# Performance work log

Hardware: AMD Instinct MI355X
Metric: run time of the kernel (lower is better)

The kernel has to match this reference:

```python
import jax, jax.numpy as jnp
import numpy as np

LN_EPS = 1e-5  # torch.nn.LayerNorm default

def g(x):
    # minGRU activation: x + 0.5 for x >= 0, sigmoid(x) otherwise (always positive)
    return jnp.where(x >= 0, x + 0.5, jax.nn.sigmoid(x))

def log_g(x):
    return jnp.where(x >= 0, jnp.log(jax.nn.relu(x) + 0.5), -jax.nn.softplus(-x))

def layernorm(x, gamma, beta):
    mu = jnp.mean(x, axis=-1, keepdims=True)
    var = jnp.var(x, axis=-1, keepdims=True)
    return (x - mu) * jax.lax.rsqrt(var + LN_EPS) * gamma + beta

def mingru_scan(gate, hidden, h0):
    # gate, hidden: (B,S,D); h0: (B,1,D) positive
    # z = sigmoid(gate); h_t = (1-z_t)*h_{t-1} + z_t * g(hidden_t)
    # evaluated via Heinsen parallel scan in log space
    log_z = -jax.nn.softplus(-gate)          # log sigmoid(gate)
    log_coeffs = -jax.nn.softplus(gate)      # log(1 - sigmoid(gate))
    log_h0 = jnp.log(h0)                     # (B,1,D)
    log_tilde_h = log_g(hidden)
    a_star = jnp.cumsum(
        jnp.concatenate([jnp.zeros_like(log_h0), log_coeffs], axis=1), axis=1
    )                                        # (B,S+1,D)
    log_vals = jnp.concatenate([log_h0, log_z + log_tilde_h], axis=1) - a_star
    log_h = a_star + jax.lax.cumlogsumexp(log_vals, axis=1)
    return jnp.exp(log_h)[:, 1:]             # (B,S,D)

def setup_inputs() -> dict:
    key = jax.random.key(0)
    k1, k2 = jax.random.split(key)
    B, S, D, L = 8, 4096, 1024, 3
    x = jax.random.normal(k1, (B, S, D), dtype=jnp.float32)
    W = jax.random.normal(k2, (L, D, 2 * D), dtype=jnp.float32) * 0.02
    b = jnp.zeros((L, 2 * D), dtype=jnp.float32)
    ln_gamma = jnp.ones((L, D), dtype=jnp.float32)
    ln_beta = jnp.zeros((L, D), dtype=jnp.float32)
    return {"x": x, "ln_gamma": ln_gamma, "ln_beta": ln_beta, "W": W, "b": b}

def reference(x, ln_gamma, ln_beta, W, b):
    B, S, D = x.shape
    L = W.shape[0]
    inp = x
    next_hidden = []
    for l in range(L):
        h_prev = jnp.full((B, 1, D), 0.5, dtype=x.dtype)  # g(zeros) = 0.5
        xn = layernorm(inp, ln_gamma[l], ln_beta[l])
        gh = jnp.einsum('bsd,de->bse', xn, W[l]) + b[l]   # (B,S,2D)
        gate, hidden = jnp.split(gh, 2, axis=2)
        out = mingru_scan(gate, hidden, h_prev)
        next_hidden.append(out[:, -1:])
        out = out + inp  # residual (sizes equal -> identity res_align)
        inp = out
    return (out, *next_hidden)
```

## Files before the change

kernel.cpp:

```cpp
#include <hip/hip_runtime.h>

typedef unsigned short u16;
typedef unsigned int   u32;
typedef float  f32x2  __attribute__((ext_vector_type(2)));
typedef float  f32x4  __attribute__((ext_vector_type(4)));
typedef short  bf16x8 __attribute__((ext_vector_type(8)));
typedef u16    u16x4  __attribute__((ext_vector_type(4)));
typedef u32    u32x4  __attribute__((ext_vector_type(4)));

#define BQ 8
#define SQ 4096
#define DQ 1024
#define NQ 2048
#define MQ 32768
#define KQ 1024
#define CCH 128
#define TCH 32
#define NT 16

__device__ __forceinline__ float bf2f(u16 u){
  union { u32 i; float f; } v; v.i = ((u32)u) << 16; return v.f;
}
__device__ __forceinline__ u16 f2bf(float f){
  union { float f; u32 i; } v; v.f = f;
  u32 r = v.i + 0x7fffu + ((v.i >> 16) & 1u);
  return (u16)(r >> 16);
}

__device__ __forceinline__ void sig_ab(float gate, float hid, float& a, float& bv){
  float eg = __expf(gate);
  float a_ = __builtin_amdgcn_rcpf(1.f + eg);
  float z  = 1.f - a_;
  float eh = __expf(hid);
  float sg = eh * __builtin_amdgcn_rcpf(1.f + eh);
  float gval = (hid >= 0.f) ? (hid + 0.5f) : sg;
  a = a_; bv = z * gval;
}

__device__ __forceinline__ void gload_lds16(const u16* g, u16* l){
  __builtin_amdgcn_global_load_lds(
      (const __attribute__((address_space(1))) u32*)g,
      (__attribute__((address_space(3)))       u32*)l,
      16, 0, 0);
}

__global__ __launch_bounds__(256) void wt_cast(const float* __restrict__ W,
                                               u16* __restrict__ WT){
  __shared__ float t[64][65];
  const int l  = blockIdx.z;
  const int k0 = blockIdx.x << 6, n0 = blockIdx.y << 6;
  const float* Wl = W  + (size_t)l * KQ * NQ;
  u16*         Tl = WT + (size_t)l * NQ * KQ;
  const int c = threadIdx.x & 63, r4 = threadIdx.x >> 6;
  #pragma unroll
  for (int i = 0; i < 16; ++i){
    int r = i * 4 + r4;
    t[r][c] = Wl[(size_t)(k0 + r) * NQ + n0 + c];
  }
  __syncthreads();
  #pragma unroll
  for (int i = 0; i < 16; ++i){
    int r = i * 4 + r4;
    Tl[(size_t)(n0 + r) * KQ + k0 + c] = f2bf(t[c][r]);
  }
}

__global__ __launch_bounds__(256) void ln_cast(const float* __restrict__ x,
                                               const float* __restrict__ gamma,
                                               const float* __restrict__ beta,
                                               u16* __restrict__ xn){
  const size_t row = blockIdx.x;
  const int tid = threadIdx.x;
  f32x4 xv = *(const f32x4*)(x + row * DQ + tid * 4);
  float s  = xv[0] + xv[1] + xv[2] + xv[3];
  float s2 = xv[0]*xv[0] + xv[1]*xv[1] + xv[2]*xv[2] + xv[3]*xv[3];
  #pragma unroll
  for (int off = 32; off > 0; off >>= 1){
    s  += __shfl_down(s,  off);
    s2 += __shfl_down(s2, off);
  }
  __shared__ float red[8];
  const int wave = tid >> 6, lane = tid & 63;
  if (lane == 0){ red[wave] = s; red[4 + wave] = s2; }
  __syncthreads();
  s  = red[0] + red[1] + red[2] + red[3];
  s2 = red[4] + red[5] + red[6] + red[7];
  const float mean = s * (1.f / DQ);
  float var = fmaxf(s2 * (1.f / DQ) - mean * mean, 0.f);
  const float rstd = rsqrtf(var + 1e-5f);
  f32x4 gv = *(const f32x4*)(gamma + tid * 4);
  f32x4 bv = *(const f32x4*)(beta  + tid * 4);
  u16x4 o;
  #pragma unroll
  for (int e = 0; e < 4; ++e) o[e] = f2bf((xv[e] - mean) * rstd * gv[e] + bv[e]);
  *(u16x4*)(xn + row * DQ + tid * 4) = o;
}

__global__ __launch_bounds__(512, 2) void gemm_k8(const u16* __restrict__ A,
                                                  const u16* __restrict__ Bt,
                                                  const float* __restrict__ bias,
                                                  u32* __restrict__ abv,
                                                  float* __restrict__ pq){
  __shared__ u16 lds[2][2][2][8192];
  const int bid = blockIdx.x;
  const int swz = ((bid & 7) << 7) | (bid >> 3);
  const int bn = swz & 7, bm = swz >> 3;
  const int m0 = bm << 8;
  const int tid = threadIdx.x;
  const int w = tid >> 6, lane = tid & 63;
  const int wr = w >> 2, wc = w & 3;
  const int lr = lane & 15, hi = lane >> 4;
  const int sl8 = lane >> 3;
  const int sslot = (lane & 7) ^ sl8;

  f32x4 acc[2][2][4][2] = {};
  bf16x8 afrA[4][2], afrB[4][2];
  bf16x8 bf0[2][2], bf1[2][2];

#define FENCE asm volatile("" ::: "memory")
#define BAR do { FENCE; __builtin_amdgcn_s_barrier(); FENCE; } while(0)
#define SB  __builtin_amdgcn_sched_barrier(0)

#define STAGE(op, hf, kt, pb_) do {                                            \
    const u16* gsrc_ = (op) ? Bt : A;                                          \
    const int rb_ = (op) ? ((bn << 7) + (hf) * 1024) : (m0 + ((hf) << 7));     \
    _Pragma("unroll")                                                          \
    for (int g_ = 0; g_ < 2; ++g_){                                            \
      const int row_ = (w << 4) + (g_ << 3) + sl8;                             \
      gload_lds16(gsrc_ + (size_t)(rb_ + row_) * KQ + ((kt) << 6) + (sslot << 3),\
                  &lds[pb_][op][hf][((w << 4) + (g_ << 3)) << 6]);             \
    }                                                                          \
  } while(0)

#define LDSRD(dst, base_, row_, slot_) do {                                    \
    const int r_ = (row_);                                                     \
    dst = *(const bf16x8*)((const char*)(base_) +                              \
          ((r_ << 7) + ((((slot_)) ^ (r_ & 7)) << 4)));                        \
  } while(0)

#define RD_A(dst, hf, buf_) do {                                               \
    const u16* Ah_ = &lds[buf_][0][hf][0];                                     \
    _Pragma("unroll")                                                          \
    for (int i_ = 0; i_ < 4; ++i_)                                             \
      _Pragma("unroll")                                                        \
      for (int kk_ = 0; kk_ < 2; ++kk_)                                        \
        LDSRD(dst[i_][kk_], Ah_, (wr << 6) + (i_ << 4) + lr, (kk_ << 2) + hi); \
  } while(0)

#define RD_B(dst, hf, buf_) do {                                               \
    const u16* Bh_ = &lds[buf_][1][hf][0];                                     \
    _Pragma("unroll")                                                          \
    for (int j_ = 0; j_ < 2; ++j_)                                             \
      _Pragma("unroll")                                                        \
      for (int kk_ = 0; kk_ < 2; ++kk_)                                        \
        LDSRD(dst[j_][kk_], Bh_, (wc << 5) + (j_ << 4) + lr, (kk_ << 2) + hi); \
  } while(0)

#define MM(qm, qn, AR, B) do {                                                 \
    SB;                                                                        \
    __builtin_amdgcn_s_setprio(1);                                             \
    _Pragma("unroll")                                                          \
    for (int kk_ = 0; kk_ < 2; ++kk_)                                          \
      _Pragma("unroll")                                                        \
      for (int i_ = 0; i_ < 4; ++i_)                                           \
        _Pragma("unroll")                                                      \
        for (int j_ = 0; j_ < 2; ++j_)                                         \
          acc[qm][qn][i_][j_] = __builtin_amdgcn_mfma_f32_16x16x32_bf16(       \
              AR[i_][kk_], B[j_][kk_], acc[qm][qn][i_][j_], 0, 0, 0);          \
    __builtin_amdgcn_s_setprio(0);                                             \
  } while(0)

  STAGE(1, 0, 0, 0); STAGE(0, 0, 0, 0); STAGE(1, 1, 0, 0); STAGE(0, 1, 0, 0);
  asm volatile("s_waitcnt vmcnt(4)" ::: "memory");
  BAR;
  RD_A(afrA, 0, 0); RD_B(bf0, 0, 0);

  for (int t = 0; t < NT; ++t){
    const int pb = t & 1, qb = pb ^ 1;
    const bool s = (t + 1 < NT);
    asm volatile("s_waitcnt vmcnt(2)" ::: "memory");
    BAR;
    if (s) STAGE(1, 0, t + 1, qb);
    RD_B(bf1, 1, pb);
    MM(0, 0, afrA, bf0);
    if (s) { asm volatile("s_waitcnt vmcnt(2)" ::: "memory"); }
    else   { asm volatile("s_waitcnt vmcnt(0)" ::: "memory"); }
    BAR;
    if (s) STAGE(0, 0, t + 1, qb);
    RD_A(afrB, 1, pb);
    MM(0, 1, afrA, bf1);
    if (s) STAGE(1, 1, t + 1, qb);
    MM(1, 0, afrB, bf0);
    if (s){
      asm volatile("s_waitcnt vmcnt(2)" ::: "memory");
      BAR;
      STAGE(0, 1, t + 1, qb);
      RD_A(afrA, 0, qb); RD_B(bf0, 0, qb);
    }
    MM(1, 1, afrB, bf1);
  }
#undef MM
#undef RD_B
#undef RD_A
#undef LDSRD
#undef STAGE
#undef SB

  const int dbase = (bn << 7) + (wc << 5) + lr;
  #pragma unroll
  for (int qm = 0; qm < 2; ++qm){
    const int row00 = m0 + (qm << 7) + (wr << 6);
    #pragma unroll
    for (int half = 0; half < 2; ++half){
      float chP[2] = {1.f, 1.f}, chQ[2] = {0.f, 0.f};
      #pragma unroll
      for (int ii = 0; ii < 2; ++ii){
        const int i = (half << 1) + ii;
        float sgP[2] = {1.f, 1.f}, sgQ[2] = {0.f, 0.f};
        #pragma unroll
        for (int r = 0; r < 4; ++r){
          const int row = row00 + (i << 4) + (hi << 2) + r;
          #pragma unroll
          for (int j = 0; j < 2; ++j){
            const int d = dbase + (j << 4);
            float gate = acc[qm][0][i][j][r] + bias[d];
            float hid  = acc[qm][1][i][j][r] + bias[1024 + d];
            float a, bv; sig_ab(gate, hid, a, bv);
            u32 pk;
            asm volatile("v_cvt_pk_bf16_f32 %0, %1, %2"
                         : "=v"(pk) : "v"(a), "v"(bv));
            abv[(size_t)row * 1024 + d] = pk;
            union { u32 u; float f; } ua, ub;
            ua.u = pk << 16; ub.u = pk & 0xffff0000u;
            sgQ[j] = ua.f * sgQ[j] + ub.f;
            sgP[j] *= ua.f;
          }
        }
        #pragma unroll
        for (int j = 0; j < 2; ++j){
          float p = sgP[j], q = sgQ[j];
          float p1 = __shfl_up(p, 16), q1 = __shfl_up(q, 16);
          if (hi >= 1){ q = p * q1 + q; p = p * p1; }
          float p2 = __shfl_up(p, 32), q2 = __shfl_up(q, 32);
          if (hi >= 2){ q = p * q2 + q; p = p * p2; }
          chQ[j] = p * chQ[j] + q;
          chP[j] = p * chP[j];
        }
      }
      if (hi == 3){
        const int rowb = row00 + (half << 5);
        const int bq = rowb >> 12, cq = (rowb >> 5) & (CCH - 1);
        #pragma unroll
        for (int j = 0; j < 2; ++j){
          const int d = dbase + (j << 4);
          f32x2 v; v[0] = chP[j]; v[1] = chQ[j];
          *(f32x2*)(pq + ((((size_t)(bq * CCH + cq)) << 10) + d) * 2) = v;
        }
      }
    }
  }
#undef BAR
#undef FENCE
}

__global__ __launch_bounds__(256) void scan2(const float* __restrict__ pq,
                                             float* __restrict__ hst,
                                             float* __restrict__ hlast){
  const int idx = blockIdx.x * 256 + threadIdx.x;
  const int b = idx >> 10, d = idx & 1023;
  float h = 0.5f;
  for (int c = 0; c < CCH; ++c){
    const size_t o = ((size_t)(b * CCH + c) << 10) + d;
    hst[o] = h;
    f32x2 v = *(const f32x2*)(pq + o * 2);
    h = v[0] * h + v[1];
  }
  hlast[idx] = h;
}

template<int MODE>
__global__ __launch_bounds__(256) void scan3f(const u32* __restrict__ abv,
                                              const float* __restrict__ hst,
                                              const void* __restrict__ inp,
                                              void* __restrict__ outp,
                                              u16* __restrict__ xn,
                                              const float* __restrict__ gamma,
                                              const float* __restrict__ beta){
  const int b = blockIdx.x >> 7;
  const int c = blockIdx.x & (CCH - 1);
  const int tid = threadIdx.x;
  const int d4 = tid << 2;
  const int wave = tid >> 6, lane = tid & 63;
  const size_t srow = (size_t)b * SQ + (size_t)c * TCH;
  const u32* base = abv + srow * 1024 + d4;
  const size_t o = ((size_t)blockIdx.x << 10) + d4;
  f32x4 h0v = *(const f32x4*)(hst + o);
  float h[4] = {h0v[0], h0v[1], h0v[2], h0v[3]};
  __shared__ float red[2][8];
  f32x4 gv = {}, bvv = {};
  if (MODE != 2){
    gv  = *(const f32x4*)(gamma + d4);
    bvv = *(const f32x4*)(beta  + d4);
  }
  for (int t = 0; t < TCH; ++t){
    u32x4 ab = *(const u32x4*)(base + (size_t)t * 1024);
    f32x4 iv;
    if (MODE == 0){
      iv = *(const f32x4*)((const float*)inp + (srow + t) * DQ + d4);
    } else {
      u16x4 ib = *(const u16x4*)((const u16*)inp + (srow + t) * DQ + d4);
      #pragma unroll
      for (int e = 0; e < 4; ++e) iv[e] = bf2f(ib[e]);
    }
    f32x4 ov;
    #pragma unroll
    for (int e = 0; e < 4; ++e){
      const float a  = bf2f((u16)(ab[e] & 0xffffu));
      const float bv = bf2f((u16)(ab[e] >> 16));
      h[e] = a * h[e] + bv;
      ov[e] = h[e] + iv[e];
    }
    if (MODE == 2){
      *(f32x4*)((float*)outp + (srow + t) * DQ + d4) = ov;
    } else {
      u16x4 ob;
      #pragma unroll
      for (int e = 0; e < 4; ++e) ob[e] = f2bf(ov[e]);
      *(u16x4*)((u16*)outp + (srow + t) * DQ + d4) = ob;
      float s  = ov[0] + ov[1] + ov[2] + ov[3];
      float s2 = ov[0]*ov[0] + ov[1]*ov[1] + ov[2]*ov[2] + ov[3]*ov[3];
      #pragma unroll
      for (int off = 32; off > 0; off >>= 1){
        s  += __shfl_down(s,  off);
        s2 += __shfl_down(s2, off);
      }
      const int rb = t & 1;
      if (lane == 0){ red[rb][wave] = s; red[rb][4 + wave] = s2; }
      __syncthreads();
      s  = red[rb][0] + red[rb][1] + red[rb][2] + red[rb][3];
      s2 = red[rb][4] + red[rb][5] + red[rb][6] + red[rb][7];
      const float mean = s * (1.f / DQ);
      float var = fmaxf(s2 * (1.f / DQ) - mean * mean, 0.f);
      const float rstd = rsqrtf(var + 1e-5f);
      u16x4 xo;
      #pragma unroll
      for (int e = 0; e < 4; ++e)
        xo[e] = f2bf((ov[e] - mean) * rstd * gv[e] + bvv[e]);
      *(u16x4*)(xn + (srow + t) * DQ + d4) = xo;
    }
  }
}

extern "C" void kernel_launch(void* const* d_in, const int* in_sizes, int n_in,
                              void* d_out, int out_size, void* d_ws, size_t ws_size,
                              hipStream_t stream) {
  const float* x     = (const float*)d_in[0];
  const float* gamma = (const float*)d_in[1];
  const float* beta  = (const float*)d_in[2];
  const float* W     = (const float*)d_in[3];
  const float* bias  = (const float*)d_in[4];
  float* out = (float*)d_out;

  char* ws = (char*)d_ws;
  const size_t ACT = (size_t)MQ * DQ * 4;
  u16*   bufA = (u16*)(ws);
  u16*   bufB = (u16*)(ws + ACT);
  u32*   abv  = (u32*)(ws + 2 * ACT);
  u16*   xn   = (u16*)(ws + 3 * ACT);
  u16*   WT   = (u16*)(ws + 3 * ACT + (size_t)MQ * DQ * 2);
  float* pq   = (float*)(ws + 3 * ACT + (size_t)MQ * DQ * 2 + (size_t)3 * NQ * KQ * 2);
  float* hst  = pq + (size_t)2 * BQ * CCH * DQ;

  wt_cast<<<dim3(KQ / 64, NQ / 64, 3), 256, 0, stream>>>(W, WT);

  const dim3 ggrid((NQ / 256) * (MQ / 256));
  ln_cast<<<MQ, 256, 0, stream>>>(x, gamma, beta, xn);
  gemm_k8<<<ggrid, 512, 0, stream>>>(xn, WT, bias, abv, pq);
  scan2<<<(BQ * DQ) / 256, 256, 0, stream>>>(pq, hst, out + (size_t)MQ * DQ);
  scan3f<0><<<BQ * CCH, 256, 0, stream>>>(abv, hst, x, bufA, xn,
                                          gamma + DQ, beta + DQ);
  gemm_k8<<<ggrid, 512, 0, stream>>>(xn, WT + (size_t)NQ * KQ, bias + NQ,
                                     abv, pq);
  scan2<<<(BQ * DQ) / 256, 256, 0, stream>>>(pq, hst,
                                             out + (size_t)MQ * DQ + BQ * DQ);
  scan3f<1><<<BQ * CCH, 256, 0, stream>>>(abv, hst, bufA, bufB, xn,
                                          gamma + 2 * DQ, beta + 2 * DQ);
  gemm_k8<<<ggrid, 512, 0, stream>>>(xn, WT + (size_t)2 * NQ * KQ, bias + 2 * NQ,
                                     abv, pq);
  scan2<<<(BQ * DQ) / 256, 256, 0, stream>>>(pq, hst,
                                             out + (size_t)MQ * DQ + 2 * BQ * DQ);
  scan3f<2><<<BQ * CCH, 256, 0, stream>>>(abv, hst, bufB, out, nullptr,
                                          nullptr, nullptr);
}
```

Before: 716.1 us.

## Interleave gate/hidden weight columns and shrink GEMM to 128x128 tiles with 4 waves

The weight transpose now interleaves gate and hidden columns in 16-wide groups, so one 128-column B tile holds both the gate and the hidden outputs for 64 channels. The GEMM is rewritten from a 256x256 tile with 8 waves and quadrant-staged LDS to a 128x128 tile with 4 waves, a simpler two-phase K-half pipeline, and a new LDS swizzle. This launches four times as many blocks and drops the complex quadrant ping-pong scheduling, at the cost of lower arithmetic intensity per block and more global traffic for A and B.

```diff
diff --git a/kernel.cpp b/kernel.cpp
--- a/kernel.cpp
+++ b/kernel.cpp
@@ -61,7 +61,10 @@
   #pragma unroll
   for (int i = 0; i < 16; ++i){
     int r = i * 4 + r4;
-    Tl[(size_t)(n0 + r) * KQ + k0 + c] = f2bf(t[c][r]);
+    const int n = n0 + r;
+    const int d = n & 1023, ishid = n >> 10;
+    const int np = ((d >> 4) << 5) + (ishid << 4) + (d & 15);
+    Tl[(size_t)np * KQ + k0 + c] = f2bf(t[c][r]);
   }
 }
 
@@ -96,166 +99,141 @@
   *(u16x4*)(xn + row * DQ + tid * 4) = o;
 }
 
-__global__ __launch_bounds__(512, 2) void gemm_k8(const u16* __restrict__ A,
+__global__ __launch_bounds__(256, 2) void gemm_k2(const u16* __restrict__ A,
                                                   const u16* __restrict__ Bt,
                                                   const float* __restrict__ bias,
                                                   u32* __restrict__ abv,
                                                   float* __restrict__ pq){
-  __shared__ u16 lds[2][2][2][8192];
+  __shared__ u16 lds[2][2][2][4096];
   const int bid = blockIdx.x;
-  const int swz = ((bid & 7) << 7) | (bid >> 3);
-  const int bn = swz & 7, bm = swz >> 3;
-  const int m0 = bm << 8;
+  const int swz = ((bid & 7) << 9) | (bid >> 3);
+  const int bn = swz & 15, bm = swz >> 4;
+  const int m0 = bm << 7;
   const int tid = threadIdx.x;
   const int w = tid >> 6, lane = tid & 63;
-  const int wr = w >> 2, wc = w & 3;
+  const int wr = w >> 1, wc = w & 1;
   const int lr = lane & 15, hi = lane >> 4;
-  const int sl8 = lane >> 3;
-  const int sslot = (lane & 7) ^ sl8;
-
-  f32x4 acc[2][2][4][2] = {};
-  bf16x8 afrA[4][2], afrB[4][2];
-  bf16x8 bf0[2][2], bf1[2][2];
+  const int sw = (hi ^ ((lr >> 1) & 3)) << 4;
+
+  f32x4 acc[4][4] = {};
+  bf16x8 af[4], bf[4];
 
 #define FENCE asm volatile("" ::: "memory")
 #define BAR do { FENCE; __builtin_amdgcn_s_barrier(); FENCE; } while(0)
-#define SB  __builtin_amdgcn_sched_barrier(0)
-
-#define STAGE(op, hf, kt, pb_) do {                                            \
+
+#define STAGE(op, kh, kt, pb_) do {                                            \
     const u16* gsrc_ = (op) ? Bt : A;                                          \
-    const int rb_ = (op) ? ((bn << 7) + (hf) * 1024) : (m0 + ((hf) << 7));     \
+    const int rb_ = (op) ? (bn << 7) : m0;                                     \
     _Pragma("unroll")                                                          \
     for (int g_ = 0; g_ < 2; ++g_){                                            \
-      const int row_ = (w << 4) + (g_ << 3) + sl8;                             \
-      gload_lds16(gsrc_ + (size_t)(rb_ + row_) * KQ + ((kt) << 6) + (sslot << 3),\
-                  &lds[pb_][op][hf][((w << 4) + (g_ << 3)) << 6]);             \
+      const int row_ = (g_ << 6) + (tid >> 2);                                 \
+      const int gs_  = ((tid & 3) ^ ((row_ >> 1) & 3)) << 3;                   \
+      gload_lds16(gsrc_ + (size_t)(rb_ + row_) * KQ + ((kt) << 6) +            \
+                      ((kh) << 5) + gs_,                                       \
+                  &lds[pb_][op][kh][(g_ << 11) + (w << 9)]);                   \
     }                                                                          \
   } while(0)
 
-#define LDSRD(dst, base_, row_, slot_) do {                                    \
-    const int r_ = (row_);                                                     \
-    dst = *(const bf16x8*)((const char*)(base_) +                              \
-          ((r_ << 7) + ((((slot_)) ^ (r_ & 7)) << 4)));                        \
+#define RD_A(kh, buf_) do {                                                    \
+    const char* Ah_ = (const char*)&lds[buf_][0][kh][0];                       \
+    _Pragma("unroll")                                                          \
+    for (int i_ = 0; i_ < 4; ++i_)                                             \
+      af[i_] = *(const bf16x8*)(Ah_ + (((wr << 6) + (i_ << 4) + lr) << 6) + sw);\
   } while(0)
 
-#define RD_A(dst, hf, buf_) do {                                               \
-    const u16* Ah_ = &lds[buf_][0][hf][0];                                     \
+#define RD_B(kh, buf_) do {                                                    \
+    const char* Bh_ = (const char*)&lds[buf_][1][kh][0];                       \
+    _Pragma("unroll")                                                          \
+    for (int j_ = 0; j_ < 4; ++j_)                                             \
+      bf[j_] = *(const bf16x8*)(Bh_ + (((wc << 6) + (j_ << 4) + lr) << 6) + sw);\
+  } while(0)
+
+#define MM do {                                                                \
+    __builtin_amdgcn_s_setprio(1);                                             \
     _Pragma("unroll")                                                          \
     for (int i_ = 0; i_ < 4; ++i_)                                             \
       _Pragma("unroll")                                                        \
-      for (int kk_ = 0; kk_ < 2; ++kk_)                                        \
-        LDSRD(dst[i_][kk_], Ah_, (wr << 6) + (i_ << 4) + lr, (kk_ << 2) + hi); \
-  } while(0)
-
-#define RD_B(dst, hf, buf_) do {                                               \
-    const u16* Bh_ = &lds[buf_][1][hf][0];                                     \
-    _Pragma("unroll")                                                          \
-    for (int j_ = 0; j_ < 2; ++j_)                                             \
-      _Pragma("unroll")                                                        \
-      for (int kk_ = 0; kk_ < 2; ++kk_)                                        \
-        LDSRD(dst[j_][kk_], Bh_, (wc << 5) + (j_ << 4) + lr, (kk_ << 2) + hi); \
-  } while(0)
-
-#define MM(qm, qn, AR, B) do {                                                 \
-    SB;                                                                        \
-    __builtin_amdgcn_s_setprio(1);                                             \
-    _Pragma("unroll")                                                          \
-    for (int kk_ = 0; kk_ < 2; ++kk_)                                          \
-      _Pragma("unroll")                                                        \
-      for (int i_ = 0; i_ < 4; ++i_)                                           \
-        _Pragma("unroll")                                                      \
-        for (int j_ = 0; j_ < 2; ++j_)                                         \
-          acc[qm][qn][i_][j_] = __builtin_amdgcn_mfma_f32_16x16x32_bf16(       \
-              AR[i_][kk_], B[j_][kk_], acc[qm][qn][i_][j_], 0, 0, 0);          \
+      for (int j_ = 0; j_ < 4; ++j_)                                           \
+        acc[i_][j_] = __builtin_amdgcn_mfma_f32_16x16x32_bf16(                 \
+            af[i_], bf[j_], acc[i_][j_], 0, 0, 0);                             \
     __builtin_amdgcn_s_setprio(0);                                             \
   } while(0)
 
-  STAGE(1, 0, 0, 0); STAGE(0, 0, 0, 0); STAGE(1, 1, 0, 0); STAGE(0, 1, 0, 0);
-  asm volatile("s_waitcnt vmcnt(4)" ::: "memory");
-  BAR;
-  RD_A(afrA, 0, 0); RD_B(bf0, 0, 0);
+  STAGE(0, 0, 0, 0); STAGE(0, 1, 0, 0); STAGE(1, 0, 0, 0); STAGE(1, 1, 0, 0);
 
   for (int t = 0; t < NT; ++t){
     const int pb = t & 1, qb = pb ^ 1;
     const bool s = (t + 1 < NT);
     asm volatile("s_waitcnt vmcnt(2)" ::: "memory");
     BAR;
-    if (s) STAGE(1, 0, t + 1, qb);
-    RD_B(bf1, 1, pb);
-    MM(0, 0, afrA, bf0);
-    if (s) { asm volatile("s_waitcnt vmcnt(2)" ::: "memory"); }
+    if (s){ STAGE(0, 0, t + 1, qb); STAGE(0, 1, t + 1, qb); }
+    RD_A(0, pb); RD_B(0, pb);
+    MM;
+    if (s) { asm volatile("s_waitcnt vmcnt(4)" ::: "memory"); }
     else   { asm volatile("s_waitcnt vmcnt(0)" ::: "memory"); }
     BAR;
-    if (s) STAGE(0, 0, t + 1, qb);
-    RD_A(afrB, 1, pb);
-    MM(0, 1, afrA, bf1);
-    if (s) STAGE(1, 1, t + 1, qb);
-    MM(1, 0, afrB, bf0);
-    if (s){
-      asm volatile("s_waitcnt vmcnt(2)" ::: "memory");
-      BAR;
-      STAGE(0, 1, t + 1, qb);
-      RD_A(afrA, 0, qb); RD_B(bf0, 0, qb);
-    }
-    MM(1, 1, afrB, bf1);
+    if (s){ STAGE(1, 0, t + 1, qb); STAGE(1, 1, t + 1, qb); }
+    RD_A(1, pb); RD_B(1, pb);
+    MM;
   }
 #undef MM
 #undef RD_B
 #undef RD_A
-#undef LDSRD
 #undef STAGE
-#undef SB
-
-  const int dbase = (bn << 7) + (wc << 5) + lr;
-  #pragma unroll
-  for (int qm = 0; qm < 2; ++qm){
-    const int row00 = m0 + (qm << 7) + (wr << 6);
+
+  const int dbase = (bn << 6) + (wc << 5) + lr;
+  float bg[2], bh[2];
+  #pragma unroll
+  for (int jp = 0; jp < 2; ++jp){
+    bg[jp] = bias[dbase + (jp << 4)];
+    bh[jp] = bias[1024 + dbase + (jp << 4)];
+  }
+  const int row00 = m0 + (wr << 6);
+  #pragma unroll
+  for (int half = 0; half < 2; ++half){
+    float chP[2] = {1.f, 1.f}, chQ[2] = {0.f, 0.f};
     #pragma unroll
-    for (int half = 0; half < 2; ++half){
-      float chP[2] = {1.f, 1.f}, chQ[2] = {0.f, 0.f};
-      #pragma unroll
-      for (int ii = 0; ii < 2; ++ii){
-        const int i = (half << 1) + ii;
-        float sgP[2] = {1.f, 1.f}, sgQ[2] = {0.f, 0.f};
+    for (int ii = 0; ii < 2; ++ii){
+      const int i = (half << 1) + ii;
+      float sgP[2] = {1.f, 1.f}, sgQ[2] = {0.f, 0.f};
+      #pragma unroll
+      for (int r = 0; r < 4; ++r){
+        const int row = row00 + (i << 4) + (hi << 2) + r;
         #pragma unroll
-        for (int r = 0; r < 4; ++r){
-          const int row = row00 + (i << 4) + (hi << 2) + r;
-          #pragma unroll
-          for (int j = 0; j < 2; ++j){
-            const int d = dbase + (j << 4);
-            float gate = acc[qm][0][i][j][r] + bias[d];
-            float hid  = acc[qm][1][i][j][r] + bias[1024 + d];
-            float a, bv; sig_ab(gate, hid, a, bv);
-            u32 pk;
-            asm volatile("v_cvt_pk_bf16_f32 %0, %1, %2"
-                         : "=v"(pk) : "v"(a), "v"(bv));
-            abv[(size_t)row * 1024 + d] = pk;
-            union { u32 u; float f; } ua, ub;
-            ua.u = pk << 16; ub.u = pk & 0xffff0000u;
-            sgQ[j] = ua.f * sgQ[j] + ub.f;
-            sgP[j] *= ua.f;
-          }
-        }
-        #pragma unroll
-        for (int j = 0; j < 2; ++j){
-          float p = sgP[j], q = sgQ[j];
-          float p1 = __shfl_up(p, 16), q1 = __shfl_up(q, 16);
-          if (hi >= 1){ q = p * q1 + q; p = p * p1; }
-          float p2 = __shfl_up(p, 32), q2 = __shfl_up(q, 32);
-          if (hi >= 2){ q = p * q2 + q; p = p * p2; }
-          chQ[j] = p * chQ[j] + q;
-          chP[j] = p * chP[j];
+        for (int jp = 0; jp < 2; ++jp){
+          const int d = dbase + (jp << 4);
+          float gate = acc[i][jp << 1][r]       + bg[jp];
+          float hid  = acc[i][(jp << 1) + 1][r] + bh[jp];
+          float a, bv; sig_ab(gate, hid, a, bv);
+          u32 pk;
+          asm volatile("v_cvt_pk_bf16_f32 %0, %1, %2"
+                       : "=v"(pk) : "v"(a), "v"(bv));
+          abv[(size_t)row * 1024 + d] = pk;
+          union { u32 u; float f; } ua, ub;
+          ua.u = pk << 16; ub.u = pk & 0xffff0000u;
+          sgQ[jp] = ua.f * sgQ[jp] + ub.f;
+          sgP[jp] *= ua.f;
         }
       }
-      if (hi == 3){
-        const int rowb = row00 + (half << 5);
-        const int bq = rowb >> 12, cq = (rowb >> 5) & (CCH - 1);
-        #pragma unroll
-        for (int j = 0; j < 2; ++j){
-          const int d = dbase + (j << 4);
-          f32x2 v; v[0] = chP[j]; v[1] = chQ[j];
-          *(f32x2*)(pq + ((((size_t)(bq * CCH + cq)) << 10) + d) * 2) = v;
-        }
+      #pragma unroll
+      for (int jp = 0; jp < 2; ++jp){
+        float p = sgP[jp], q = sgQ[jp];
+        float p1 = __shfl_up(p, 16), q1 = __shfl_up(q, 16);
+        if (hi >= 1){ q = p * q1 + q; p = p * p1; }
+        float p2 = __shfl_up(p, 32), q2 = __shfl_up(q, 32);
+        if (hi >= 2){ q = p * q2 + q; p = p * p2; }
+        chQ[jp] = p * chQ[jp] + q;
+        chP[jp] = p * chP[jp];
+      }
+    }
+    if (hi == 3){
+      const int rowb = row00 + (half << 5);
+      const int bq = rowb >> 12, cq = (rowb >> 5) & (CCH - 1);
+      #pragma unroll
+      for (int jp = 0; jp < 2; ++jp){
+        const int d = dbase + (jp << 4);
+        f32x2 v; v[0] = chP[jp]; v[1] = chQ[jp];
+        *(f32x2*)(pq + ((((size_t)(bq * CCH + cq)) << 10) + d) * 2) = v;
       }
     }
   }
@@ -373,19 +351,19 @@
 
   wt_cast<<<dim3(KQ / 64, NQ / 64, 3), 256, 0, stream>>>(W, WT);
 
-  const dim3 ggrid((NQ / 256) * (MQ / 256));
+  const dim3 ggrid(16 * (MQ / 128));
   ln_cast<<<MQ, 256, 0, stream>>>(x, gamma, beta, xn);
-  gemm_k8<<<ggrid, 512, 0, stream>>>(xn, WT, bias, abv, pq);
+  gemm_k2<<<ggrid, 256, 0, stream>>>(xn, WT, bias, abv, pq);
   scan2<<<(BQ * DQ) / 256, 256, 0, stream>>>(pq, hst, out + (size_t)MQ * DQ);
   scan3f<0><<<BQ * CCH, 256, 0, stream>>>(abv, hst, x, bufA, xn,
                                           gamma + DQ, beta + DQ);
-  gemm_k8<<<ggrid, 512, 0, stream>>>(xn, WT + (size_t)NQ * KQ, bias + NQ,
+  gemm_k2<<<ggrid, 256, 0, stream>>>(xn, WT + (size_t)NQ * KQ, bias + NQ,
                                      abv, pq);
   scan2<<<(BQ * DQ) / 256, 256, 0, stream>>>(pq, hst,
                                              out + (size_t)MQ * DQ + BQ * DQ);
   scan3f<1><<<BQ * CCH, 256, 0, stream>>>(abv, hst, bufA, bufB, xn,
                                           gamma + 2 * DQ, beta + 2 * DQ);
-  gemm_k8<<<ggrid, 512, 0, stream>>>(xn, WT + (size_t)2 * NQ * KQ, bias + 2 * NQ,
+  gemm_k2<<<ggrid, 256, 0, stream>>>(xn, WT + (size_t)2 * NQ * KQ, bias + 2 * NQ,
                                      abv, pq);
   scan2<<<(BQ * DQ) / 256, 256, 0, stream>>>(pq, hst,
                                              out + (size_t)MQ * DQ + 2 * BQ * DQ);
```

New measurement: 806.6 us. +12.7%, slower.
